# Kernel optimization log

Measured on AMD Instinct MI355X. Metric: run time of the kernel, lower is better.

Reference implementation:

```python
import jax, jax.numpy as jnp
import numpy as np

BLOCK_SIZE = 256
NEG = -10000.0  # matches the module's additive mask constant (not -inf)

def setup_inputs() -> dict:
    key = jax.random.key(0)
    qkv = jax.random.normal(key, (4, 4096, 192), dtype=jnp.float32)
    return {"qkv": qkv}

def reference(qkv):
    B, S, dm = qkv.shape
    d = dm // 3
    q, k, v = qkv[..., :d], qkv[..., d:2*d], qkv[..., 2*d:]
    scale = 1.0 / jnp.sqrt(jnp.asarray(d, dtype=qkv.dtype))
    scores = jnp.einsum('bqd,bkd->bqk', q, k * scale)  # [B,S,S]
    i = jnp.arange(S)[:, None]
    j = jnp.arange(S)[None, :]
    # allowed: i - block_size <= j <= i ; else additive -10000 (as in torch code)
    mask = jnp.where((j <= i) & (j >= i - BLOCK_SIZE), 0.0, NEG).astype(scores.dtype)
    attn = jax.nn.softmax(scores + mask[None, :, :], axis=-1)
    return jnp.einsum('bqk,bkd->bqd', attn, v)
```

## Files before the change

kernel.cpp:

```cpp
#include <hip/hip_runtime.h>
#include <hip/hip_bf16.h>


#define LOG2E 1.4426950408889634f

typedef __attribute__((ext_vector_type(8))) short  frag;
typedef __attribute__((ext_vector_type(4))) float  f32x4;

static __device__ inline short f2bf(float x) {
    __hip_bfloat16 h = __float2bfloat16(x);
    return __builtin_bit_cast(short, h);
}

#define LSTR 72

__global__ __launch_bounds__(256) void swa_mfma(const float* __restrict__ qkv,
                                                float* __restrict__ out)
{
    __shared__ short Qs[64 * LSTR];
    __shared__ short Ks[64 * LSTR];
    __shared__ short Vt[64 * LSTR];
    __shared__ short Pw[4][16 * LSTR];

    const int b    = blockIdx.y;
    const int q0   = blockIdx.x * 64;
    const int t    = threadIdx.x;
    const int w    = t >> 6;
    const int lane = t & 63;
    const int cl   = lane & 15;
    const int quad = lane >> 4;

    const float4* qkv4 = (const float4*)qkv;
    const int r_st  = t >> 2;
    const int c4_st = t & 3;

    {
        const size_t base = (size_t)(b * 4096 + q0 + r_st) * 48;
        #pragma unroll
        for (int i = 0; i < 4; ++i) {
            float4 v = qkv4[base + c4_st + 4 * i];
            short4 s4 = { f2bf(v.x * 0.125f), f2bf(v.y * 0.125f),
                          f2bf(v.z * 0.125f), f2bf(v.w * 0.125f) };
            *(short4*)&Qs[r_st * LSTR + 4 * (c4_st + 4 * i)] = s4;
        }
    }

    const int c0 = (q0 >= 256) ? 0 : (4 - (q0 >> 6));

    float4 preK[4], preV[4];
    {
        const int kb = q0 - 256 + 64 * c0;
        const size_t base = (size_t)(b * 4096 + kb + r_st) * 48;
        #pragma unroll
        for (int i = 0; i < 4; ++i) {
            preK[i] = qkv4[base + 16 + c4_st + 4 * i];
            preV[i] = qkv4[base + 32 + c4_st + 4 * i];
        }
    }

    __syncthreads();
    const frag qf0 = *(const frag*)&Qs[(16 * w + cl) * LSTR + 8 * quad];
    const frag qf1 = *(const frag*)&Qs[(16 * w + cl) * LSTR + 32 + 8 * quad];

    float m[4], l[4];
    f32x4 oacc[4];
    #pragma unroll
    for (int r = 0; r < 4; ++r) { m[r] = -1e30f; l[r] = 0.f; }
    #pragma unroll
    for (int t4 = 0; t4 < 4; ++t4) oacc[t4] = (f32x4){0.f, 0.f, 0.f, 0.f};

    const int ql = 4 * quad;

    for (int c = c0; c < 5; ++c) {
        __syncthreads();

        #pragma unroll
        for (int i = 0; i < 4; ++i) {
            short4 k4 = { f2bf(preK[i].x), f2bf(preK[i].y),
                          f2bf(preK[i].z), f2bf(preK[i].w) };
            *(short4*)&Ks[r_st * LSTR + 4 * (c4_st + 4 * i)] = k4;
            const int d0 = 4 * (c4_st + 4 * i);
            Vt[(d0 + 0) * LSTR + r_st] = f2bf(preV[i].x);
            Vt[(d0 + 1) * LSTR + r_st] = f2bf(preV[i].y);
            Vt[(d0 + 2) * LSTR + r_st] = f2bf(preV[i].z);
            Vt[(d0 + 3) * LSTR + r_st] = f2bf(preV[i].w);
        }
        __syncthreads();

        if (c < 4) {
            const int kb = q0 - 256 + 64 * (c + 1);
            const size_t base = (size_t)(b * 4096 + kb + r_st) * 48;
            #pragma unroll
            for (int i = 0; i < 4; ++i) {
                preK[i] = qkv4[base + 16 + c4_st + 4 * i];
                preV[i] = qkv4[base + 32 + c4_st + 4 * i];
            }
        }

        f32x4 sc[4];
        #pragma unroll
        for (int t4 = 0; t4 < 4; ++t4) sc[t4] = (f32x4){0.f, 0.f, 0.f, 0.f};
        #pragma unroll
        for (int t4 = 0; t4 < 4; ++t4) {
            const frag kf0 = *(const frag*)&Ks[(16 * t4 + cl) * LSTR + 8 * quad];
            const frag kf1 = *(const frag*)&Ks[(16 * t4 + cl) * LSTR + 32 + 8 * quad];
            sc[t4] = __builtin_amdgcn_mfma_f32_16x16x32_bf16(qf0, kf0, sc[t4], 0, 0, 0);
            sc[t4] = __builtin_amdgcn_mfma_f32_16x16x32_bf16(qf1, kf1, sc[t4], 0, 0, 0);
        }

        if (c == 4) {
            #pragma unroll
            for (int t4 = 0; t4 < 4; ++t4)
                #pragma unroll
                for (int r = 0; r < 4; ++r)
                    if (16 * w + ql + r < 16 * t4 + cl) sc[t4][r] = -1e30f;
        } else if (c == 0) {
            #pragma unroll
            for (int t4 = 0; t4 < 4; ++t4)
                #pragma unroll
                for (int r = 0; r < 4; ++r)
                    if (16 * w + ql + r > 16 * t4 + cl) sc[t4][r] = -1e30f;
        }

        #pragma unroll
        for (int r = 0; r < 4; ++r) {
            float mx = fmaxf(fmaxf(sc[0][r], sc[1][r]), fmaxf(sc[2][r], sc[3][r]));
            #pragma unroll
            for (int off = 1; off < 16; off <<= 1) mx = fmaxf(mx, __shfl_xor(mx, off));
            const float mnew  = fmaxf(m[r], mx);
            const float alpha = __builtin_amdgcn_exp2f((m[r] - mnew) * LOG2E);
            m[r] = mnew;
            float sum = 0.f;
            #pragma unroll
            for (int t4 = 0; t4 < 4; ++t4) {
                float p = __builtin_amdgcn_exp2f((sc[t4][r] - mnew) * LOG2E);
                Pw[w][(ql + r) * LSTR + 16 * t4 + cl] = f2bf(p);
                sum += p;
            }
            #pragma unroll
            for (int off = 1; off < 16; off <<= 1) sum += __shfl_xor(sum, off);
            l[r] = l[r] * alpha + sum;
            #pragma unroll
            for (int t4 = 0; t4 < 4; ++t4) oacc[t4][r] *= alpha;
        }

        const frag pf0 = *(const frag*)&Pw[w][cl * LSTR + 8 * quad];
        const frag pf1 = *(const frag*)&Pw[w][cl * LSTR + 32 + 8 * quad];
        #pragma unroll
        for (int t4 = 0; t4 < 4; ++t4) {
            const frag vf0 = *(const frag*)&Vt[(16 * t4 + cl) * LSTR + 8 * quad];
            const frag vf1 = *(const frag*)&Vt[(16 * t4 + cl) * LSTR + 32 + 8 * quad];
            oacc[t4] = __builtin_amdgcn_mfma_f32_16x16x32_bf16(pf0, vf0, oacc[t4], 0, 0, 0);
            oacc[t4] = __builtin_amdgcn_mfma_f32_16x16x32_bf16(pf1, vf1, oacc[t4], 0, 0, 0);
        }
    }

    #pragma unroll
    for (int r = 0; r < 4; ++r) {
        const float inv = 1.0f / l[r];
        const size_t row = (size_t)(b * 4096 + q0 + 16 * w + ql + r) * 64;
        #pragma unroll
        for (int t4 = 0; t4 < 4; ++t4)
            out[row + 16 * t4 + cl] = oacc[t4][r] * inv;
    }
}

extern "C" void kernel_launch(void* const* d_in, const int* in_sizes, int n_in,
                              void* d_out, int out_size, void* d_ws, size_t ws_size,
                              hipStream_t stream) {
    const float* qkv = (const float*)d_in[0];
    float* out = (float*)d_out;
    dim3 grid(64, 4);
    dim3 block(256);
    hipLaunchKernelGGL(swa_mfma, grid, block, 0, stream, qkv, out);
}
```

Baseline: 69.71 us.

## Split key tiles across two wave groups with split-softmax merge, DPP reductions

Doubles the block to 512 threads. Each 64-key tile is split between two groups of four waves, each group handling 32 keys per query strip, so each wave issues half the QK and PV MFMAs. At the end the two groups' partial outputs, maxima and sums are merged through shared memory. Row reductions switch from shfl_xor to DPP moves, and masked scores skip the exp. This adds an extra merge pass, more shared memory and a final sync. The grid stays at 256 blocks, so per-block latency should drop but redundant loads stay the same.

```diff
diff --git a/kernel.cpp b/kernel.cpp
--- a/kernel.cpp
+++ b/kernel.cpp
@@ -12,74 +12,97 @@
     return __builtin_bit_cast(short, h);
 }
 
+#define DPPF(x, ctrl) __builtin_bit_cast(float, \
+    __builtin_amdgcn_mov_dpp(__builtin_bit_cast(int, (x)), (ctrl), 0xF, 0xF, true))
+
+static __device__ inline float red16_max(float x) {
+    x = fmaxf(x, DPPF(x, 0xB1));
+    x = fmaxf(x, DPPF(x, 0x4E));
+    x = fmaxf(x, DPPF(x, 0x141));
+    x = fmaxf(x, DPPF(x, 0x140));
+    return x;
+}
+static __device__ inline float red16_sum(float x) {
+    x += DPPF(x, 0xB1);
+    x += DPPF(x, 0x4E);
+    x += DPPF(x, 0x141);
+    x += DPPF(x, 0x140);
+    return x;
+}
+
 #define LSTR 72
-
-__global__ __launch_bounds__(256) void swa_mfma(const float* __restrict__ qkv,
-                                                float* __restrict__ out)
+#define PSTR 40
+#define OSTR 65
+
+__global__ __launch_bounds__(512, 2) void swa_mfma2(const float* __restrict__ qkv,
+                                                    float* __restrict__ out)
 {
     __shared__ short Qs[64 * LSTR];
     __shared__ short Ks[64 * LSTR];
     __shared__ short Vt[64 * LSTR];
-    __shared__ short Pw[4][16 * LSTR];
+    __shared__ short Pw[8][16 * PSTR];
+    __shared__ float Om[4][16 * OSTR];
+    __shared__ float2 mlbuf[4][16];
 
     const int b    = blockIdx.y;
     const int q0   = blockIdx.x * 64;
     const int t    = threadIdx.x;
     const int w    = t >> 6;
+    const int s    = w & 3;
+    const int g    = w >> 2;
     const int lane = t & 63;
     const int cl   = lane & 15;
     const int quad = lane >> 4;
+    const int ql   = 4 * quad;
 
     const float4* qkv4 = (const float4*)qkv;
-    const int r_st  = t >> 2;
-    const int c4_st = t & 3;
+    const int r_st = t >> 3;
+    const int c8   = t & 7;
 
     {
         const size_t base = (size_t)(b * 4096 + q0 + r_st) * 48;
         #pragma unroll
-        for (int i = 0; i < 4; ++i) {
-            float4 v = qkv4[base + c4_st + 4 * i];
+        for (int i = 0; i < 2; ++i) {
+            float4 v = qkv4[base + c8 + 8 * i];
             short4 s4 = { f2bf(v.x * 0.125f), f2bf(v.y * 0.125f),
                           f2bf(v.z * 0.125f), f2bf(v.w * 0.125f) };
-            *(short4*)&Qs[r_st * LSTR + 4 * (c4_st + 4 * i)] = s4;
+            *(short4*)&Qs[r_st * LSTR + 4 * (c8 + 8 * i)] = s4;
         }
     }
 
     const int c0 = (q0 >= 256) ? 0 : (4 - (q0 >> 6));
 
-    float4 preK[4], preV[4];
+    float4 preK[2], preV[2];
     {
         const int kb = q0 - 256 + 64 * c0;
         const size_t base = (size_t)(b * 4096 + kb + r_st) * 48;
         #pragma unroll
-        for (int i = 0; i < 4; ++i) {
-            preK[i] = qkv4[base + 16 + c4_st + 4 * i];
-            preV[i] = qkv4[base + 32 + c4_st + 4 * i];
+        for (int i = 0; i < 2; ++i) {
+            preK[i] = qkv4[base + 16 + c8 + 8 * i];
+            preV[i] = qkv4[base + 32 + c8 + 8 * i];
         }
     }
 
     __syncthreads();
-    const frag qf0 = *(const frag*)&Qs[(16 * w + cl) * LSTR + 8 * quad];
-    const frag qf1 = *(const frag*)&Qs[(16 * w + cl) * LSTR + 32 + 8 * quad];
+    const frag qf0 = *(const frag*)&Qs[(16 * s + cl) * LSTR + 8 * quad];
+    const frag qf1 = *(const frag*)&Qs[(16 * s + cl) * LSTR + 32 + 8 * quad];
 
     float m[4], l[4];
     f32x4 oacc[4];
     #pragma unroll
     for (int r = 0; r < 4; ++r) { m[r] = -1e30f; l[r] = 0.f; }
     #pragma unroll
-    for (int t4 = 0; t4 < 4; ++t4) oacc[t4] = (f32x4){0.f, 0.f, 0.f, 0.f};
-
-    const int ql = 4 * quad;
+    for (int n4 = 0; n4 < 4; ++n4) oacc[n4] = (f32x4){0.f, 0.f, 0.f, 0.f};
 
     for (int c = c0; c < 5; ++c) {
         __syncthreads();
 
         #pragma unroll
-        for (int i = 0; i < 4; ++i) {
+        for (int i = 0; i < 2; ++i) {
             short4 k4 = { f2bf(preK[i].x), f2bf(preK[i].y),
                           f2bf(preK[i].z), f2bf(preK[i].w) };
-            *(short4*)&Ks[r_st * LSTR + 4 * (c4_st + 4 * i)] = k4;
-            const int d0 = 4 * (c4_st + 4 * i);
+            *(short4*)&Ks[r_st * LSTR + 4 * (c8 + 8 * i)] = k4;
+            const int d0 = 4 * (c8 + 8 * i);
             Vt[(d0 + 0) * LSTR + r_st] = f2bf(preV[i].x);
             Vt[(d0 + 1) * LSTR + r_st] = f2bf(preV[i].y);
             Vt[(d0 + 2) * LSTR + r_st] = f2bf(preV[i].z);
@@ -91,77 +114,97 @@
             const int kb = q0 - 256 + 64 * (c + 1);
             const size_t base = (size_t)(b * 4096 + kb + r_st) * 48;
             #pragma unroll
-            for (int i = 0; i < 4; ++i) {
-                preK[i] = qkv4[base + 16 + c4_st + 4 * i];
-                preV[i] = qkv4[base + 32 + c4_st + 4 * i];
-            }
-        }
-
-        f32x4 sc[4];
-        #pragma unroll
-        for (int t4 = 0; t4 < 4; ++t4) sc[t4] = (f32x4){0.f, 0.f, 0.f, 0.f};
-        #pragma unroll
-        for (int t4 = 0; t4 < 4; ++t4) {
+            for (int i = 0; i < 2; ++i) {
+                preK[i] = qkv4[base + 16 + c8 + 8 * i];
+                preV[i] = qkv4[base + 32 + c8 + 8 * i];
+            }
+        }
+
+        f32x4 sc[2];
+        #pragma unroll
+        for (int u = 0; u < 2; ++u) {
+            const int t4 = 2 * g + u;
+            sc[u] = (f32x4){0.f, 0.f, 0.f, 0.f};
             const frag kf0 = *(const frag*)&Ks[(16 * t4 + cl) * LSTR + 8 * quad];
             const frag kf1 = *(const frag*)&Ks[(16 * t4 + cl) * LSTR + 32 + 8 * quad];
-            sc[t4] = __builtin_amdgcn_mfma_f32_16x16x32_bf16(qf0, kf0, sc[t4], 0, 0, 0);
-            sc[t4] = __builtin_amdgcn_mfma_f32_16x16x32_bf16(qf1, kf1, sc[t4], 0, 0, 0);
+            sc[u] = __builtin_amdgcn_mfma_f32_16x16x32_bf16(qf0, kf0, sc[u], 0, 0, 0);
+            sc[u] = __builtin_amdgcn_mfma_f32_16x16x32_bf16(qf1, kf1, sc[u], 0, 0, 0);
         }
 
         if (c == 4) {
             #pragma unroll
-            for (int t4 = 0; t4 < 4; ++t4)
+            for (int u = 0; u < 2; ++u) {
+                const int t4 = 2 * g + u;
                 #pragma unroll
                 for (int r = 0; r < 4; ++r)
-                    if (16 * w + ql + r < 16 * t4 + cl) sc[t4][r] = -1e30f;
+                    if (16 * s + ql + r < 16 * t4 + cl) sc[u][r] = -1e30f;
+            }
         } else if (c == 0) {
             #pragma unroll
-            for (int t4 = 0; t4 < 4; ++t4)
+            for (int u = 0; u < 2; ++u) {
+                const int t4 = 2 * g + u;
                 #pragma unroll
                 for (int r = 0; r < 4; ++r)
-                    if (16 * w + ql + r > 16 * t4 + cl) sc[t4][r] = -1e30f;
+                    if (16 * s + ql + r > 16 * t4 + cl) sc[u][r] = -1e30f;
+            }
         }
 
         #pragma unroll
         for (int r = 0; r < 4; ++r) {
-            float mx = fmaxf(fmaxf(sc[0][r], sc[1][r]), fmaxf(sc[2][r], sc[3][r]));
-            #pragma unroll
-            for (int off = 1; off < 16; off <<= 1) mx = fmaxf(mx, __shfl_xor(mx, off));
+            float mx = red16_max(fmaxf(sc[0][r], sc[1][r]));
             const float mnew  = fmaxf(m[r], mx);
             const float alpha = __builtin_amdgcn_exp2f((m[r] - mnew) * LOG2E);
             m[r] = mnew;
             float sum = 0.f;
             #pragma unroll
-            for (int t4 = 0; t4 < 4; ++t4) {
-                float p = __builtin_amdgcn_exp2f((sc[t4][r] - mnew) * LOG2E);
-                Pw[w][(ql + r) * LSTR + 16 * t4 + cl] = f2bf(p);
+            for (int u = 0; u < 2; ++u) {
+                float p = (sc[u][r] <= -1e29f)
+                            ? 0.f
+                            : __builtin_amdgcn_exp2f((sc[u][r] - mnew) * LOG2E);
+                Pw[w][(ql + r) * PSTR + 16 * u + cl] = f2bf(p);
                 sum += p;
             }
-            #pragma unroll
-            for (int off = 1; off < 16; off <<= 1) sum += __shfl_xor(sum, off);
-            l[r] = l[r] * alpha + sum;
-            #pragma unroll
-            for (int t4 = 0; t4 < 4; ++t4) oacc[t4][r] *= alpha;
-        }
-
-        const frag pf0 = *(const frag*)&Pw[w][cl * LSTR + 8 * quad];
-        const frag pf1 = *(const frag*)&Pw[w][cl * LSTR + 32 + 8 * quad];
-        #pragma unroll
-        for (int t4 = 0; t4 < 4; ++t4) {
-            const frag vf0 = *(const frag*)&Vt[(16 * t4 + cl) * LSTR + 8 * quad];
-            const frag vf1 = *(const frag*)&Vt[(16 * t4 + cl) * LSTR + 32 + 8 * quad];
-            oacc[t4] = __builtin_amdgcn_mfma_f32_16x16x32_bf16(pf0, vf0, oacc[t4], 0, 0, 0);
-            oacc[t4] = __builtin_amdgcn_mfma_f32_16x16x32_bf16(pf1, vf1, oacc[t4], 0, 0, 0);
-        }
-    }
-
-    #pragma unroll
-    for (int r = 0; r < 4; ++r) {
-        const float inv = 1.0f / l[r];
-        const size_t row = (size_t)(b * 4096 + q0 + 16 * w + ql + r) * 64;
-        #pragma unroll
-        for (int t4 = 0; t4 < 4; ++t4)
-            out[row + 16 * t4 + cl] = oacc[t4][r] * inv;
+            l[r] = l[r] * alpha + red16_sum(sum);
+            #pragma unroll
+            for (int n4 = 0; n4 < 4; ++n4) oacc[n4][r] *= alpha;
+        }
+
+        const frag pf = *(const frag*)&Pw[w][cl * PSTR + 8 * quad];
+        #pragma unroll
+        for (int n4 = 0; n4 < 4; ++n4) {
+            const frag vf = *(const frag*)&Vt[(16 * n4 + cl) * LSTR + 32 * g + 8 * quad];
+            oacc[n4] = __builtin_amdgcn_mfma_f32_16x16x32_bf16(pf, vf, oacc[n4], 0, 0, 0);
+        }
+    }
+
+    if (g == 1) {
+        #pragma unroll
+        for (int n4 = 0; n4 < 4; ++n4)
+            #pragma unroll
+            for (int r = 0; r < 4; ++r)
+                Om[s][(ql + r) * OSTR + 16 * n4 + cl] = oacc[n4][r];
+        if (cl == 0)
+            #pragma unroll
+            for (int r = 0; r < 4; ++r)
+                mlbuf[s][ql + r] = make_float2(m[r], l[r]);
+    }
+    __syncthreads();
+    if (g == 0) {
+        #pragma unroll
+        for (int r = 0; r < 4; ++r) {
+            const float2 ml1 = mlbuf[s][ql + r];
+            const float M  = fmaxf(m[r], ml1.x);
+            const float a0 = __builtin_amdgcn_exp2f((m[r]  - M) * LOG2E);
+            const float a1 = __builtin_amdgcn_exp2f((ml1.x - M) * LOG2E);
+            const float L  = l[r] * a0 + ml1.y * a1;
+            const float inv = 1.0f / L;
+            const size_t row = (size_t)(b * 4096 + q0 + 16 * s + ql + r) * 64;
+            #pragma unroll
+            for (int n4 = 0; n4 < 4; ++n4) {
+                const float o1 = Om[s][(ql + r) * OSTR + 16 * n4 + cl];
+                out[row + 16 * n4 + cl] = (oacc[n4][r] * a0 + o1 * a1) * inv;
+            }
+        }
     }
 }
 
@@ -171,6 +214,6 @@
     const float* qkv = (const float*)d_in[0];
     float* out = (float*)d_out;
     dim3 grid(64, 4);
-    dim3 block(256);
-    hipLaunchKernelGGL(swa_mfma, grid, block, 0, stream, qkv, out);
-}
+    dim3 block(512);
+    hipLaunchKernelGGL(swa_mfma2, grid, block, 0, stream, qkv, out);
+}
```

New measurement: 67.60 us. -3.0%, faster.
